# Kernel optimization log

Measured on AMD Instinct MI355X. Metric: run time of the kernel, lower is better.

Reference implementation:

```python
import jax, jax.numpy as jnp
import numpy as np
import math

N_HEADS = 16
FACTOR = 5

def setup_inputs() -> dict:
    key = jax.random.key(0)
    ks = jax.random.split(key, 9)
    B, T, D = 4, 2048, 1024
    w = lambda k: jax.random.normal(k, (D, D), dtype=jnp.float32) * 0.02
    return {
        "x": jax.random.normal(ks[0], (B, T, D), dtype=jnp.float32),
        "Wq": w(ks[1]), "bq": jnp.zeros((D,), jnp.float32),
        "Wk": w(ks[2]), "bk": jnp.zeros((D,), jnp.float32),
        "Wv": w(ks[3]), "bv": jnp.zeros((D,), jnp.float32),
        "Wo": w(ks[4]), "bo": jnp.zeros((D,), jnp.float32),
    }

def reference(x, Wq, bq, Wk, bk, Wv, bv, Wo, bo):
    B, T, D = x.shape
    H = N_HEADS
    hd = D // H
    scale = hd ** (-0.5)

    def proj(W, b):
        # [B,T,D] -> [B,H,T,hd]
        return (x @ W + b).reshape(B, T, H, hd).transpose(0, 2, 1, 3)

    q = proj(Wq, bq)
    k = proj(Wk, bk)
    v = proj(Wv, bv)

    # top-u query selection by L1 norm per (b,h)
    u = min(int(FACTOR * math.log(T)), T)
    q_norm = jnp.sum(jnp.abs(q), axis=-1)          # [B,H,T]
    _, idx = jax.lax.top_k(q_norm, u)              # [B,H,u]

    # gather selected queries; compute only the u selected score rows
    q_sel = jnp.take_along_axis(q, idx[..., None], axis=2)  # [B,H,u,hd]
    sel_scores = jnp.einsum('bhud,bhtd->bhut', q_sel, k) * scale  # [B,H,u,T]

    # causal mask for selected rows: key pos j attends iff j <= query pos
    causal = jnp.arange(T)[None, None, None, :] <= idx[..., None]  # [B,H,u,T]
    sel_scores = jnp.where(causal, sel_scores, -jnp.inf)

    attn = jax.nn.softmax(sel_scores, axis=-1)     # dropout omitted (eval)
    sel_out = jnp.einsum('bhut,bhtd->bhud', attn, v)  # [B,H,u,hd]

    # scatter selected rows back into zeros (non-selected rows stay 0)
    bi = jnp.arange(B)[:, None, None]
    hi = jnp.arange(H)[None, :, None]
    attn_out = jnp.zeros((B, H, T, hd), x.dtype).at[bi, hi, idx].set(sel_out)

    out = attn_out.transpose(0, 2, 1, 3).reshape(B, T, D)
    return out @ Wo + bo
```

## Files before the change

kernel.cpp:

```cpp
#include <hip/hip_runtime.h>
#include <hip/hip_bf16.h>
#include <math.h>

#define B_  4
#define T_  2048
#define D_  1024
#define H_  16
#define HD_ 64
#define U_  38
#define M_  (B_*T_)
#define NCB_ 8
#define NC_ 96

typedef __attribute__((ext_vector_type(8))) short bf16x8;
typedef __attribute__((ext_vector_type(4))) float f32x4;

__device__ __forceinline__ short f2b(float f) {
    __hip_bfloat16 b = __float2bfloat16(f);
    return *(short*)&b;
}
__device__ __forceinline__ float b2f(short s) {
    __hip_bfloat16 b = *(__hip_bfloat16*)&s;
    return __bfloat162float(b);
}
__device__ __forceinline__ unsigned pack2(float lo, float hi) {
    unsigned a = (unsigned short)f2b(lo);
    unsigned b = ((unsigned)(unsigned short)f2b(hi)) << 16;
    return a | b;
}

__device__ __forceinline__ void gload16(const void* g, void* l) {
    __builtin_amdgcn_global_load_lds(
        (const __attribute__((address_space(1))) unsigned int*)g,
        (__attribute__((address_space(3))) unsigned int*)l,
        16, 0, 0);
}

__global__ __launch_bounds__(256) void conv_fused(
    const float* __restrict__ x,
    const float* __restrict__ Wq, const float* __restrict__ Wk,
    const float* __restrict__ Wv, const float* __restrict__ Wo,
    const float* __restrict__ bo,
    short* __restrict__ xh, short* __restrict__ xl,
    short* __restrict__ wq2, short* __restrict__ wkvt, short* __restrict__ wot,
    float* __restrict__ out)
{
    __shared__ float tile[32][33];
    const int bid = blockIdx.x;
    if (bid < 8192) {
        const size_t i = ((size_t)bid * 256 + threadIdx.x) * 4;
        float4 v = *(const float4*)(x + i);
        short4 h, l;
        h.x = f2b(v.x); l.x = f2b(v.x - b2f(h.x));
        h.y = f2b(v.y); l.y = f2b(v.y - b2f(h.y));
        h.z = f2b(v.z); l.z = f2b(v.z - b2f(h.z));
        h.w = f2b(v.w); l.w = f2b(v.w - b2f(h.w));
        *(short4*)(xh + i) = h;
        *(short4*)(xl + i) = l;
        return;
    }
    if (bid >= 12288) {
        const size_t i = (size_t)(bid - 12288) * 256 + threadIdx.x;
        float4 bv = *(const float4*)(bo + ((i & 255) << 2));
        *(float4*)(out + i * 4) = bv;
        return;
    }
    const int q = bid - 8192;
    const int which = q >> 10;
    const int by = (q & 1023) >> 5, bx = q & 31;
    const float* W = which == 0 ? Wq : (which == 1 ? Wk : (which == 2 ? Wv : Wo));
    const int k0 = by * 32, n0 = bx * 32;
    const int tx = threadIdx.x & 31, ty = threadIdx.x >> 5;
    #pragma unroll
    for (int r = ty; r < 32; r += 8)
        tile[r][tx] = W[(size_t)(k0 + r) * D_ + n0 + tx];
    __syncthreads();
    #pragma unroll
    for (int r = ty; r < 32; r += 8) {
        float v = tile[tx][r];
        size_t o = (size_t)(n0 + r) * D_ + k0 + tx;
        if (which == 0) {
            short h = f2b(v);
            wq2[o] = h;
            wq2[o + 1048576] = f2b(v - b2f(h));
        } else if (which == 3) {
            wot[o] = f2b(v);
        } else {
            wkvt[(size_t)(which - 1) * D_ * D_ + o] = f2b(v);
        }
    }
}

__global__ __launch_bounds__(256) void gemm_fused(
    const short* __restrict__ xh, const short* __restrict__ wq2,
    const short* __restrict__ wkvt,
    const float* __restrict__ bq, const float* __restrict__ bk,
    const float* __restrict__ bv,
    float* __restrict__ qnorm, short* __restrict__ kb, short* __restrict__ vt)
{
    __shared__ short As[128 * 64];
    __shared__ short Bs[128 * 64];
    const int bid = blockIdx.x;
    const bool isQ = bid < 512;
    const int tid = threadIdx.x, wid = tid >> 6, lane = tid & 63;
    const int l15 = lane & 15, gr = lane >> 4;
    const int lb = isQ ? bid : bid - 512;
    const int m0 = (lb & 63) * 128;
    const int n0 = (lb >> 6) * 128;
    const bool isK = !isQ && (n0 < D_);
    const int wr = (wid >> 1) * 64, wc = (wid & 1) * 64;

    f32x4 acc[4][4];
    #pragma unroll
    for (int i = 0; i < 4; ++i)
        #pragma unroll
        for (int j = 0; j < 4; ++j)
            acc[i][j] = (f32x4){0.f, 0.f, 0.f, 0.f};

    const short* Asrc = xh;
    const short* Bsrc = isQ ? wq2 : wkvt;

    for (int kt = 0; kt < 16; ++kt) {
        const int ka = kt * 64;
        #pragma unroll
        for (int i = 0; i < 4; ++i) {
            const int e = tid + i * 256;
            const int row = e >> 3;
            const int soff = ((e & 7) ^ (row & 7)) * 8;
            gload16(Asrc + (size_t)(m0 + row) * D_ + ka + soff,
                    (char*)As + i * 4096 + wid * 1024);
            gload16(Bsrc + (size_t)(n0 + row) * D_ + ka + soff,
                    (char*)Bs + i * 4096 + wid * 1024);
        }
        __syncthreads();
        #pragma unroll
        for (int ks = 0; ks < 2; ++ks) {
            bf16x8 a[4], b[4];
            #pragma unroll
            for (int i = 0; i < 4; ++i)
                a[i] = *(bf16x8*)((char*)As + (wr + i * 16 + l15) * 128
                                   + (((ks << 2) | gr) ^ (l15 & 7)) * 16);
            #pragma unroll
            for (int j = 0; j < 4; ++j)
                b[j] = *(bf16x8*)((char*)Bs + (wc + j * 16 + l15) * 128
                                   + (((ks << 2) | gr) ^ (l15 & 7)) * 16);
            if (isK) {
                #pragma unroll
                for (int i = 0; i < 4; ++i)
                    #pragma unroll
                    for (int j = 0; j < 4; ++j)
                        acc[i][j] = __builtin_amdgcn_mfma_f32_16x16x32_bf16(b[j], a[i], acc[i][j], 0, 0, 0);
            } else {
                #pragma unroll
                for (int i = 0; i < 4; ++i)
                    #pragma unroll
                    for (int j = 0; j < 4; ++j)
                        acc[i][j] = __builtin_amdgcn_mfma_f32_16x16x32_bf16(a[i], b[j], acc[i][j], 0, 0, 0);
            }
        }
        __syncthreads();
    }

    if (isQ) {
        const int h = (n0 + wc) >> 6;
        #pragma unroll
        for (int i = 0; i < 4; ++i)
            #pragma unroll
            for (int r = 0; r < 4; ++r) {
                int row = m0 + wr + i * 16 + gr * 4 + r;
                float s = 0.f;
                #pragma unroll
                for (int j = 0; j < 4; ++j) {
                    int col = n0 + wc + j * 16 + l15;
                    s += fabsf(acc[i][j][r] + bq[col]);
                }
                s += __shfl_xor(s, 1);
                s += __shfl_xor(s, 2);
                s += __shfl_xor(s, 4);
                s += __shfl_xor(s, 8);
                if (l15 == 0) {
                    int b = row >> 11, t = row & (T_ - 1);
                    qnorm[((size_t)b * H_ + h) * T_ + t] = s;
                }
            }
    } else if (isK) {
        #pragma unroll
        for (int i = 0; i < 4; ++i)
            #pragma unroll
            for (int j = 0; j < 4; ++j) {
                const int m = m0 + wr + i * 16 + l15;
                const int bb = m >> 11, t = m & (T_ - 1);
                const int n = n0 + wc + j * 16 + gr * 4;
                const int hh = n >> 6, dd = n & 63;
                float4 bias = *(const float4*)(bk + n);
                short4 pk;
                pk.x = f2b(acc[i][j][0] + bias.x);
                pk.y = f2b(acc[i][j][1] + bias.y);
                pk.z = f2b(acc[i][j][2] + bias.z);
                pk.w = f2b(acc[i][j][3] + bias.w);
                *(short4*)(kb + (((size_t)bb * H_ + hh) * T_ + t) * HD_ + dd) = pk;
            }
    } else {
        #pragma unroll
        for (int i = 0; i < 4; ++i)
            #pragma unroll
            for (int j = 0; j < 4; ++j) {
                const int col = n0 + wc + j * 16 + l15;
                const int rowb = m0 + wr + i * 16 + gr * 4;
                const int bb = rowb >> 11, t0 = rowb & (T_ - 1);
                const int cc2 = col - D_;
                const int hh = cc2 >> 6, dd = cc2 & 63;
                const float bias = bv[cc2];
                short4 pk;
                pk.x = f2b(acc[i][j][0] + bias);
                pk.y = f2b(acc[i][j][1] + bias);
                pk.z = f2b(acc[i][j][2] + bias);
                pk.w = f2b(acc[i][j][3] + bias);
                *(short4*)(vt + (((size_t)bb * H_ + hh) * HD_ + dd) * T_ + t0) = pk;
            }
    }
}

__global__ __launch_bounds__(64) void cand_kernel(
    const float* __restrict__ qnorm, int* __restrict__ cand)
{
    const int g = blockIdx.x;
    const int lane = threadIdx.x;
    unsigned v[32];
    const float* src = qnorm + (size_t)g * T_ + lane * 32;
    #pragma unroll
    for (int i = 0; i < 32; i += 4) {
        float4 t = *(const float4*)(src + i);
        v[i] = __float_as_uint(t.x); v[i + 1] = __float_as_uint(t.y);
        v[i + 2] = __float_as_uint(t.z); v[i + 3] = __float_as_uint(t.w);
    }
    unsigned lo = 0, hi = 0x7F800000u;
    while (lo < hi) {
        unsigned mid = lo + ((hi - lo) >> 1);
        int c = 0;
        #pragma unroll
        for (int i = 0; i < 32; ++i) c += (v[i] >= mid) ? 1 : 0;
        #pragma unroll
        for (int off = 1; off < 64; off <<= 1) c += __shfl_xor(c, off);
        if (c <= NC_) hi = mid; else lo = mid + 1;
    }
    const unsigned tau = lo;
    int myc = 0;
    #pragma unroll
    for (int i = 0; i < 32; ++i) myc += (v[i] >= tau) ? 1 : 0;
    int inc = myc;
    for (int off = 1; off < 64; off <<= 1) {
        int n = __shfl_up(inc, off);
        if (lane >= off) inc += n;
    }
    const int total = __shfl(inc, 63);
    int pos = inc - myc;
    #pragma unroll
    for (int i = 0; i < 32; ++i)
        if (v[i] >= tau) cand[g * NC_ + pos++] = lane * 32 + i;
    for (int p = total + lane; p < NC_; p += 64)
        cand[g * NC_ + p] = -1;
}

__global__ __launch_bounds__(64) void recheck_kernel(
    const short* __restrict__ xh, const short* __restrict__ xl,
    const short* __restrict__ wq2, const float* __restrict__ bq,
    const int* __restrict__ cand,
    float* __restrict__ cnorm, short* __restrict__ candq)
{
    const int blk = blockIdx.x;
    const int g = blk / 6, rt = blk % 6;
    const int b = g >> 4, h = g & 15;
    const int lane = threadIdx.x, l15 = lane & 15, gr = lane >> 4;

    const int aslot = rt * 16 + l15;
    int at = cand[g * NC_ + aslot];
    const size_t arow = ((size_t)b * T_ + (at < 0 ? 0 : at)) * D_;

    f32x4 acc[4];
    #pragma unroll
    for (int j = 0; j < 4; ++j) acc[j] = (f32x4){0.f, 0.f, 0.f, 0.f};

    const short* wqh = wq2;
    const short* wql = wq2 + 1048576;
    for (int kt = 0; kt < 32; ++kt) {
        const int k0 = kt * 32 + gr * 8;
        bf16x8 ah = *(const bf16x8*)(xh + arow + k0);
        bf16x8 al = *(const bf16x8*)(xl + arow + k0);
        #pragma unroll
        for (int j = 0; j < 4; ++j) {
            const size_t wrow = (size_t)(h * HD_ + j * 16 + l15) * D_ + k0;
            bf16x8 bh = *(const bf16x8*)(wqh + wrow);
            bf16x8 bl = *(const bf16x8*)(wql + wrow);
            acc[j] = __builtin_amdgcn_mfma_f32_16x16x32_bf16(ah, bh, acc[j], 0, 0, 0);
            acc[j] = __builtin_amdgcn_mfma_f32_16x16x32_bf16(ah, bl, acc[j], 0, 0, 0);
            acc[j] = __builtin_amdgcn_mfma_f32_16x16x32_bf16(al, bh, acc[j], 0, 0, 0);
        }
    }

    #pragma unroll
    for (int r = 0; r < 4; ++r) {
        const int slot = rt * 16 + gr * 4 + r;
        float s = 0.f;
        #pragma unroll
        for (int j = 0; j < 4; ++j) {
            const int col = j * 16 + l15;
            float val = acc[j][r] + bq[h * HD_ + col];
            candq[((size_t)g * NC_ + slot) * HD_ + col] = f2b(val);
            s += fabsf(val);
        }
        s += __shfl_xor(s, 1);
        s += __shfl_xor(s, 2);
        s += __shfl_xor(s, 4);
        s += __shfl_xor(s, 8);
        if (l15 == 0) {
            int ct = cand[g * NC_ + slot];
            cnorm[g * NC_ + slot] = (ct < 0) ? -3e38f : s;
        }
    }
}

__global__ __launch_bounds__(64) void topk38_kernel(
    const float* __restrict__ cnorm, const int* __restrict__ cand,
    int* __restrict__ idxb, int* __restrict__ slotb)
{
    const int g = blockIdx.x;
    const int lane = threadIdx.x;
    float v[2]; int tt[2];
    bool fl0 = false, fl1 = false;
    #pragma unroll
    for (int i = 0; i < 2; ++i) {
        int s = lane + 64 * i;
        if (s < NC_) {
            v[i] = cnorm[g * NC_ + s];
            int c = cand[g * NC_ + s];
            tt[i] = (c < 0) ? (1 << 30) : c;
            if (c < 0) v[i] = -3e38f;
        } else { v[i] = -3e38f; tt[i] = 1 << 30; }
    }
    for (int it = 0; it < U_; ++it) {
        float bv; int bt, bi;
        if (v[0] > v[1] || (v[0] == v[1] && tt[0] < tt[1])) { bv = v[0]; bt = tt[0]; bi = 0; }
        else { bv = v[1]; bt = tt[1]; bi = 1; }
        int bs = lane + 64 * bi;
        for (int off = 32; off; off >>= 1) {
            float ov = __shfl_xor(bv, off);
            int ot = __shfl_xor(bt, off);
            int os = __shfl_xor(bs, off);
            if (ov > bv || (ov == bv && ot < bt)) { bv = ov; bt = ot; bs = os; }
        }
        if ((bs & 63) == lane) {
            if ((bs >> 6) == 0) { v[0] = -3e38f; fl0 = true; }
            else                { v[1] = -3e38f; fl1 = true; }
        }
    }
    unsigned long long b0 = __ballot(fl0), b1 = __ballot(fl1);
    int n0 = __popcll(b0);
    unsigned long long lowmask = ((unsigned long long)1 << lane) - 1;
    if (fl0) {
        int p = __popcll(b0 & lowmask);
        idxb[g * U_ + p] = tt[0];
        slotb[g * 40 + p] = lane;
    }
    if (fl1) {
        int p = n0 + __popcll(b1 & lowmask);
        idxb[g * U_ + p] = tt[1];
        slotb[g * 40 + p] = lane + 64;
    }
}

__global__ __launch_bounds__(256) void attn_part(
    const short* __restrict__ candq, const int* __restrict__ slotb,
    const short* __restrict__ kb, const short* __restrict__ vt,
    const int* __restrict__ idxb,
    float* __restrict__ pm, float* __restrict__ pl, float* __restrict__ po)
{
    __shared__ short qs[48 * 72];
    __shared__ __align__(16) char shbuf[40448];
    __shared__ int sidx[48];
    short* pls  = (short*)shbuf;
    float* redo = (float*)shbuf;
    float* redm = (float*)(shbuf + 38912);
    float* redl = (float*)(shbuf + 39680);

    const int bid = blockIdx.x;
    const int g = bid & 63;
    const int c = bid >> 6;
    const int tid = threadIdx.x, wid = tid >> 6, lane = tid & 63;
    const int l15 = lane & 15, gr = lane >> 4;
    const int j0w = (c * 4 + wid) * 64;

    if (tid < 48) sidx[tid] = (tid < U_) ? idxb[g * U_ + tid] : 0;
    __syncthreads();
    for (int e = tid; e < 48 * 16; e += 256) {
        int u = e >> 4, d4 = e & 15;
        short4 v = make_short4(0, 0, 0, 0);
        if (u < U_) {
            int slot = slotb[g * 40 + u];
            v = *(const short4*)(candq + ((size_t)g * NC_ + slot) * HD_ + d4 * 4);
        }
        *(short4*)&qs[u * 72 + d4 * 4] = v;
    }
    __syncthreads();

    bool skp[3];
    #pragma unroll
    for (int uf = 0; uf < 3; ++uf) {
        int mi = uf * 16 + 15; if (mi >= U_) mi = U_ - 1;
        skp[uf] = (sidx[mi] < j0w);
    }

    int su[3];
    #pragma unroll
    for (int uf = 0; uf < 3; ++uf) su[uf] = sidx[uf * 16 + l15];

    f32x4 accs[3][4];
    #pragma unroll
    for (int uf = 0; uf < 3; ++uf)
        #pragma unroll
        for (int jf = 0; jf < 4; ++jf)
            accs[uf][jf] = (f32x4){0.f, 0.f, 0.f, 0.f};

    bf16x8 ka[4][2];
    #pragma unroll
    for (int jf = 0; jf < 4; ++jf)
        #pragma unroll
        for (int ks = 0; ks < 2; ++ks)
            ka[jf][ks] = *(const bf16x8*)(kb + ((size_t)g * T_ + j0w + jf * 16 + l15) * HD_ + ks * 32 + gr * 8);

    #pragma unroll
    for (int uf = 0; uf < 3; ++uf) {
        if (!skp[uf]) {
            bf16x8 q0 = *(bf16x8*)&qs[(uf * 16 + l15) * 72 + gr * 8];
            bf16x8 q1 = *(bf16x8*)&qs[(uf * 16 + l15) * 72 + 32 + gr * 8];
            #pragma unroll
            for (int jf = 0; jf < 4; ++jf) {
                accs[uf][jf] = __builtin_amdgcn_mfma_f32_16x16x32_bf16(ka[jf][0], q0, accs[uf][jf], 0, 0, 0);
                accs[uf][jf] = __builtin_amdgcn_mfma_f32_16x16x32_bf16(ka[jf][1], q1, accs[uf][jf], 0, 0, 0);
            }
        }
    }

    short* pw = pls + wid * 48 * 72;
    #pragma unroll
    for (int uf = 0; uf < 3; ++uf) {
        if (skp[uf]) {
            if (gr == 0) {
                int u = uf * 16 + l15;
                redm[wid * 48 + u] = -1e30f;
                redl[wid * 48 + u] = 0.f;
            }
        } else {
            float mm = -3e38f;
            #pragma unroll
            for (int jf = 0; jf < 4; ++jf)
                #pragma unroll
                for (int r = 0; r < 4; ++r) {
                    int j = j0w + jf * 16 + gr * 4 + r;
                    float s = accs[uf][jf][r] * 0.125f;
                    s = (j <= su[uf]) ? s : -1e30f;
                    accs[uf][jf][r] = s;
                    mm = fmaxf(mm, s);
                }
            mm = fmaxf(mm, __shfl_xor(mm, 16));
            mm = fmaxf(mm, __shfl_xor(mm, 32));
            float ll = 0.f;
            #pragma unroll
            for (int jf = 0; jf < 4; ++jf)
                #pragma unroll
                for (int r = 0; r < 4; ++r) {
                    float e = __expf(accs[uf][jf][r] - mm);
                    accs[uf][jf][r] = e;
                    ll += e;
                }
            ll += __shfl_xor(ll, 16);
            ll += __shfl_xor(ll, 32);
            if (gr == 0) {
                int u = uf * 16 + l15;
                redm[wid * 48 + u] = mm;
                redl[wid * 48 + u] = ll;
            }
            #pragma unroll
            for (int jf = 0; jf < 4; ++jf) {
                uint2 wv;
                wv.x = pack2(accs[uf][jf][0], accs[uf][jf][1]);
                wv.y = pack2(accs[uf][jf][2], accs[uf][jf][3]);
                *(uint2*)&pw[(uf * 16 + l15) * 72 + jf * 16 + gr * 4] = wv;
            }
        }
    }

    bf16x8 va[4][2];
    #pragma unroll
    for (int df = 0; df < 4; ++df)
        #pragma unroll
        for (int ks = 0; ks < 2; ++ks)
            va[df][ks] = *(const bf16x8*)(vt + ((size_t)g * HD_ + df * 16 + l15) * T_ + j0w + ks * 32 + gr * 8);

    f32x4 acco[4][3];
    #pragma unroll
    for (int df = 0; df < 4; ++df)
        #pragma unroll
        for (int uf = 0; uf < 3; ++uf)
            acco[df][uf] = (f32x4){0.f, 0.f, 0.f, 0.f};
    #pragma unroll
    for (int uf = 0; uf < 3; ++uf) {
        if (!skp[uf]) {
            bf16x8 p0 = *(bf16x8*)&pw[(uf * 16 + l15) * 72 + gr * 8];
            bf16x8 p1 = *(bf16x8*)&pw[(uf * 16 + l15) * 72 + 32 + gr * 8];
            #pragma unroll
            for (int df = 0; df < 4; ++df) {
                acco[df][uf] = __builtin_amdgcn_mfma_f32_16x16x32_bf16(va[df][0], p0, acco[df][uf], 0, 0, 0);
                acco[df][uf] = __builtin_amdgcn_mfma_f32_16x16x32_bf16(va[df][1], p1, acco[df][uf], 0, 0, 0);
            }
        }
    }

    __syncthreads();

    #pragma unroll
    for (int df = 0; df < 4; ++df)
        #pragma unroll
        for (int uf = 0; uf < 3; ++uf) {
            int u = uf * 16 + l15;
            if (u < U_) {
                float4 o;
                o.x = acco[df][uf][0]; o.y = acco[df][uf][1];
                o.z = acco[df][uf][2]; o.w = acco[df][uf][3];
                *(float4*)&redo[((size_t)(wid * 38 + u)) * 64 + df * 16 + gr * 4] = o;
            }
        }
    __syncthreads();

    for (int e = tid; e < U_ * 64; e += 256) {
        int u = e >> 6, d = e & 63;
        float m0 = redm[u], m1 = redm[48 + u], m2 = redm[96 + u], m3 = redm[144 + u];
        float m = fmaxf(fmaxf(m0, m1), fmaxf(m2, m3));
        float e0 = __expf(m0 - m), e1 = __expf(m1 - m), e2 = __expf(m2 - m), e3 = __expf(m3 - m);
        float l = redl[u] * e0 + redl[48 + u] * e1 + redl[96 + u] * e2 + redl[144 + u] * e3;
        float o = redo[(size_t)u * 64 + d] * e0
                + redo[(size_t)(38 + u) * 64 + d] * e1
                + redo[(size_t)(76 + u) * 64 + d] * e2
                + redo[(size_t)(114 + u) * 64 + d] * e3;
        po[((size_t)(g * NCB_ + c) * U_ + u) * HD_ + d] = o;
        if (d == 0) {
            pm[(size_t)(g * NCB_ + c) * U_ + u] = m;
            pl[(size_t)(g * NCB_ + c) * U_ + u] = l;
        }
    }
}

__global__ __launch_bounds__(256) void oproj_kernel(
    const float* __restrict__ pm, const float* __restrict__ pl,
    const float* __restrict__ po, const int* __restrict__ idxb,
    const short* __restrict__ wot, float* __restrict__ out)
{
    __shared__ short sel[48 * 72];
    __shared__ int st[48];
    __shared__ float swl[U_][NCB_];
    const int g = blockIdx.x;
    const int b = g >> 4, h = g & 15;
    const int tid = threadIdx.x, w = tid >> 6, lane = tid & 63;
    const int l15 = lane & 15, gr = lane >> 4;

    if (tid < 48) st[tid] = (tid < U_) ? idxb[g * U_ + tid] : 0;
    if (tid < U_) {
        float mc[NCB_], lc[NCB_];
        #pragma unroll
        for (int c = 0; c < NCB_; ++c) {
            mc[c] = pm[(size_t)(g * NCB_ + c) * U_ + tid];
            lc[c] = pl[(size_t)(g * NCB_ + c) * U_ + tid];
        }
        float m = -3e38f;
        #pragma unroll
        for (int c = 0; c < NCB_; ++c) m = fmaxf(m, mc[c]);
        float wv[NCB_], l = 0.f;
        #pragma unroll
        for (int c = 0; c < NCB_; ++c) { wv[c] = __expf(mc[c] - m); l += lc[c] * wv[c]; }
        float inv = 1.f / l;
        #pragma unroll
        for (int c = 0; c < NCB_; ++c) swl[tid][c] = wv[c] * inv;
    }
    for (int e = tid; e < 48 * 16; e += 256) {
        int u = e >> 4, d4 = e & 15;
        if (u >= U_) *(short4*)&sel[u * 72 + d4 * 4] = make_short4(0, 0, 0, 0);
    }
    __syncthreads();

    for (int e = tid; e < U_ * 64; e += 256) {
        int u = e >> 6, d = e & 63;
        float o = 0.f;
        #pragma unroll
        for (int c = 0; c < NCB_; ++c)
            o += po[((size_t)(g * NCB_ + c) * U_ + u) * HD_ + d] * swl[u][c];
        sel[u * 72 + d] = f2b(o);
    }
    __syncthreads();

    bf16x8 a[3][2];
    #pragma unroll
    for (int uf = 0; uf < 3; ++uf)
        #pragma unroll
        for (int ks = 0; ks < 2; ++ks)
            a[uf][ks] = *(bf16x8*)&sel[(uf * 16 + l15) * 72 + ks * 32 + gr * 8];

    for (int nf = 0; nf < 16; ++nf) {
        const int n0 = w * 256 + nf * 16;
        bf16x8 bf[2];
        #pragma unroll
        for (int ks = 0; ks < 2; ++ks)
            bf[ks] = *(const bf16x8*)(wot + (size_t)(n0 + l15) * D_ + h * HD_ + ks * 32 + gr * 8);
        f32x4 acc[3];
        #pragma unroll
        for (int uf = 0; uf < 3; ++uf) {
            acc[uf] = (f32x4){0.f, 0.f, 0.f, 0.f};
            acc[uf] = __builtin_amdgcn_mfma_f32_16x16x32_bf16(a[uf][0], bf[0], acc[uf], 0, 0, 0);
            acc[uf] = __builtin_amdgcn_mfma_f32_16x16x32_bf16(a[uf][1], bf[1], acc[uf], 0, 0, 0);
        }
        #pragma unroll
        for (int uf = 0; uf < 3; ++uf)
            #pragma unroll
            for (int r = 0; r < 4; ++r) {
                int u = uf * 16 + gr * 4 + r;
                if (u < U_)
                    atomicAdd(out + ((size_t)b * T_ + st[u]) * D_ + n0 + l15, acc[uf][r]);
            }
    }
}

extern "C" void kernel_launch(void* const* d_in, const int* in_sizes, int n_in,
                              void* d_out, int out_size, void* d_ws, size_t ws_size,
                              hipStream_t stream)
{
    const float* x  = (const float*)d_in[0];
    const float* Wq = (const float*)d_in[1];
    const float* bq = (const float*)d_in[2];
    const float* Wk = (const float*)d_in[3];
    const float* bk = (const float*)d_in[4];
    const float* Wv = (const float*)d_in[5];
    const float* bv = (const float*)d_in[6];
    const float* Wo = (const float*)d_in[7];
    const float* bo = (const float*)d_in[8];
    float* out = (float*)d_out;

    char* ws = (char*)d_ws;
    short* xh    = (short*)(ws);
    short* xl    = (short*)(ws + 16777216);
    short* wq2   = (short*)(ws + 33554432);
    short* wkvt  = (short*)(ws + 37748736);
    short* kb    = (short*)(ws + 41943040);
    short* vt    = (short*)(ws + 58720256);
    float* qnorm = (float*)(ws + 75497472);
    int*   idxb  = (int*)  (ws + 76021760);
    int*   cand  = (int*)  (ws + 76660736);
    float* cnorm = (float*)(ws + 76697600);
    int*   slotb = (int*)  (ws + 76734464);
    short* candq = (short*)(ws + 76750848);
    short* wot   = (short*)(ws + 77930496);
    float* po    = (float*)(ws);
    float* pm    = (float*)(ws + 19922944);
    float* pl    = (float*)(ws + 20234240);

    conv_fused<<<8192 + 4096 + 8192, 256, 0, stream>>>(x, Wq, Wk, Wv, Wo, bo,
                                                       xh, xl, wq2, wkvt, wot, out);
    gemm_fused<<<1536, 256, 0, stream>>>(xh, wq2, wkvt, bq, bk, bv, qnorm, kb, vt);
    cand_kernel<<<B_ * H_, 64, 0, stream>>>(qnorm, cand);
    recheck_kernel<<<B_ * H_ * 6, 64, 0, stream>>>(xh, xl, wq2, bq, cand, cnorm, candq);
    topk38_kernel<<<B_ * H_, 64, 0, stream>>>(cnorm, cand, idxb, slotb);
    attn_part<<<64 * NCB_, 256, 0, stream>>>(candq, slotb, kb, vt, idxb, pm, pl, po);
    oproj_kernel<<<B_ * H_, 256, 0, stream>>>(pm, pl, po, idxb, wot, out);
}
```

Measured before the change: 185.3 us.

## Drop xl buffer, split x on the fly in recheck, shrink candidate pool

The conversion kernel no longer writes the low-half bf16 residual of x for all tokens. The recheck kernel now reads fp32 x rows for its candidates and splits them into high and low bf16 parts in registers. The candidate pool drops from 96 to 64 per (batch, head), so recheck launches fewer blocks and top-k runs on a single wave register. gemm_fused also gets an occupancy hint. A smaller candidate pool raises the risk that a true top-38 query falls outside the approximate candidate set.

```diff
diff --git a/kernel.cpp b/kernel.cpp
--- a/kernel.cpp
+++ b/kernel.cpp
@@ -10,7 +10,7 @@
 #define U_  38
 #define M_  (B_*T_)
 #define NCB_ 8
-#define NC_ 96
+#define NC_ 64
 
 typedef __attribute__((ext_vector_type(8))) short bf16x8;
 typedef __attribute__((ext_vector_type(4))) float f32x4;
@@ -41,7 +41,7 @@
     const float* __restrict__ Wq, const float* __restrict__ Wk,
     const float* __restrict__ Wv, const float* __restrict__ Wo,
     const float* __restrict__ bo,
-    short* __restrict__ xh, short* __restrict__ xl,
+    short* __restrict__ xh,
     short* __restrict__ wq2, short* __restrict__ wkvt, short* __restrict__ wot,
     float* __restrict__ out)
 {
@@ -50,13 +50,9 @@
     if (bid < 8192) {
         const size_t i = ((size_t)bid * 256 + threadIdx.x) * 4;
         float4 v = *(const float4*)(x + i);
-        short4 h, l;
-        h.x = f2b(v.x); l.x = f2b(v.x - b2f(h.x));
-        h.y = f2b(v.y); l.y = f2b(v.y - b2f(h.y));
-        h.z = f2b(v.z); l.z = f2b(v.z - b2f(h.z));
-        h.w = f2b(v.w); l.w = f2b(v.w - b2f(h.w));
+        short4 h;
+        h.x = f2b(v.x); h.y = f2b(v.y); h.z = f2b(v.z); h.w = f2b(v.w);
         *(short4*)(xh + i) = h;
-        *(short4*)(xl + i) = l;
         return;
     }
     if (bid >= 12288) {
@@ -91,7 +87,7 @@
     }
 }
 
-__global__ __launch_bounds__(256) void gemm_fused(
+__global__ __launch_bounds__(256, 4) void gemm_fused(
     const short* __restrict__ xh, const short* __restrict__ wq2,
     const short* __restrict__ wkvt,
     const float* __restrict__ bq, const float* __restrict__ bk,
@@ -263,19 +259,19 @@
 }
 
 __global__ __launch_bounds__(64) void recheck_kernel(
-    const short* __restrict__ xh, const short* __restrict__ xl,
+    const float* __restrict__ x,
     const short* __restrict__ wq2, const float* __restrict__ bq,
     const int* __restrict__ cand,
     float* __restrict__ cnorm, short* __restrict__ candq)
 {
     const int blk = blockIdx.x;
-    const int g = blk / 6, rt = blk % 6;
+    const int g = blk >> 2, rt = blk & 3;
     const int b = g >> 4, h = g & 15;
     const int lane = threadIdx.x, l15 = lane & 15, gr = lane >> 4;
 
     const int aslot = rt * 16 + l15;
     int at = cand[g * NC_ + aslot];
-    const size_t arow = ((size_t)b * T_ + (at < 0 ? 0 : at)) * D_;
+    const float* xrow = x + ((size_t)b * T_ + (at < 0 ? 0 : at)) * D_;
 
     f32x4 acc[4];
     #pragma unroll
@@ -285,8 +281,16 @@
     const short* wql = wq2 + 1048576;
     for (int kt = 0; kt < 32; ++kt) {
         const int k0 = kt * 32 + gr * 8;
-        bf16x8 ah = *(const bf16x8*)(xh + arow + k0);
-        bf16x8 al = *(const bf16x8*)(xl + arow + k0);
+        float4 xa = *(const float4*)(xrow + k0);
+        float4 xb = *(const float4*)(xrow + k0 + 4);
+        float xs[8] = {xa.x, xa.y, xa.z, xa.w, xb.x, xb.y, xb.z, xb.w};
+        bf16x8 ah, al;
+        #pragma unroll
+        for (int e = 0; e < 8; ++e) {
+            short hh = f2b(xs[e]);
+            ah[e] = hh;
+            al[e] = f2b(xs[e] - b2f(hh));
+        }
         #pragma unroll
         for (int j = 0; j < 4; ++j) {
             const size_t wrow = (size_t)(h * HD_ + j * 16 + l15) * D_ + k0;
@@ -326,46 +330,27 @@
 {
     const int g = blockIdx.x;
     const int lane = threadIdx.x;
-    float v[2]; int tt[2];
-    bool fl0 = false, fl1 = false;
-    #pragma unroll
-    for (int i = 0; i < 2; ++i) {
-        int s = lane + 64 * i;
-        if (s < NC_) {
-            v[i] = cnorm[g * NC_ + s];
-            int c = cand[g * NC_ + s];
-            tt[i] = (c < 0) ? (1 << 30) : c;
-            if (c < 0) v[i] = -3e38f;
-        } else { v[i] = -3e38f; tt[i] = 1 << 30; }
-    }
+    float v = cnorm[g * NC_ + lane];
+    int c = cand[g * NC_ + lane];
+    int tt = (c < 0) ? (1 << 30) : c;
+    if (c < 0) v = -3e38f;
+    bool fl = false;
     for (int it = 0; it < U_; ++it) {
-        float bv; int bt, bi;
-        if (v[0] > v[1] || (v[0] == v[1] && tt[0] < tt[1])) { bv = v[0]; bt = tt[0]; bi = 0; }
-        else { bv = v[1]; bt = tt[1]; bi = 1; }
-        int bs = lane + 64 * bi;
+        float bv = v; int bt = tt; int bs = lane;
         for (int off = 32; off; off >>= 1) {
             float ov = __shfl_xor(bv, off);
             int ot = __shfl_xor(bt, off);
             int os = __shfl_xor(bs, off);
             if (ov > bv || (ov == bv && ot < bt)) { bv = ov; bt = ot; bs = os; }
         }
-        if ((bs & 63) == lane) {
-            if ((bs >> 6) == 0) { v[0] = -3e38f; fl0 = true; }
-            else                { v[1] = -3e38f; fl1 = true; }
-        }
-    }
-    unsigned long long b0 = __ballot(fl0), b1 = __ballot(fl1);
-    int n0 = __popcll(b0);
+        if (bs == lane) { v = -3e38f; fl = true; }
+    }
+    unsigned long long bm = __ballot(fl);
     unsigned long long lowmask = ((unsigned long long)1 << lane) - 1;
-    if (fl0) {
-        int p = __popcll(b0 & lowmask);
-        idxb[g * U_ + p] = tt[0];
+    if (fl) {
+        int p = __popcll(bm & lowmask);
+        idxb[g * U_ + p] = tt;
         slotb[g * 40 + p] = lane;
-    }
-    if (fl1) {
-        int p = n0 + __popcll(b1 & lowmask);
-        idxb[g * U_ + p] = tt[1];
-        slotb[g * 40 + p] = lane + 64;
     }
 }
 
@@ -645,7 +630,6 @@
 
     char* ws = (char*)d_ws;
     short* xh    = (short*)(ws);
-    short* xl    = (short*)(ws + 16777216);
     short* wq2   = (short*)(ws + 33554432);
     short* wkvt  = (short*)(ws + 37748736);
     short* kb    = (short*)(ws + 41943040);
@@ -662,10 +646,10 @@
     float* pl    = (float*)(ws + 20234240);
 
     conv_fused<<<8192 + 4096 + 8192, 256, 0, stream>>>(x, Wq, Wk, Wv, Wo, bo,
-                                                       xh, xl, wq2, wkvt, wot, out);
+                                                       xh, wq2, wkvt, wot, out);
     gemm_fused<<<1536, 256, 0, stream>>>(xh, wq2, wkvt, bq, bk, bv, qnorm, kb, vt);
     cand_kernel<<<B_ * H_, 64, 0, stream>>>(qnorm, cand);
-    recheck_kernel<<<B_ * H_ * 6, 64, 0, stream>>>(xh, xl, wq2, bq, cand, cnorm, candq);
+    recheck_kernel<<<B_ * H_ * 4, 64, 0, stream>>>(x, wq2, bq, cand, cnorm, candq);
     topk38_kernel<<<B_ * H_, 64, 0, stream>>>(cnorm, cand, idxb, slotb);
     attn_part<<<64 * NCB_, 256, 0, stream>>>(candq, slotb, kb, vt, idxb, pm, pl, po);
     oproj_kernel<<<B_ * H_, 256, 0, stream>>>(pm, pl, po, idxb, wot, out);
```

After: 593.6 us. 220% more time.
